# Kernel tuning notes

Measured on AMD Instinct MI355X. Metric: run time of the kernel, lower is better.

## Reference

```python
import jax, jax.numpy as jnp
import numpy as np

B, C, H, W = 8, 256, 64, 64


def setup_inputs() -> dict:
    key = jax.random.key(0)
    ks = jax.random.split(key, 9)
    s = 1.0 / np.sqrt(C)  # conv2d default init scale
    return {
        "foreground": jax.random.normal(ks[0], (B, C, H, W), jnp.float32),
        "background": jax.random.normal(ks[1], (B, C, H, W), jnp.float32),
        "mask": jax.random.uniform(ks[2], (B, C, H, W), jnp.float32),
        "Wq": jax.random.normal(ks[3], (C, C), jnp.float32) * s,
        "bq": jnp.zeros((C,), jnp.float32),
        "Wk": jax.random.normal(ks[4], (C, C), jnp.float32) * s,
        "bk": jnp.zeros((C,), jnp.float32),
        "Wv": jax.random.normal(ks[5], (C, C), jnp.float32) * s,
        "bv": jnp.zeros((C,), jnp.float32),
        "gamma": jnp.ones((1,), jnp.float32),
    }


def _conv1x1(x, Wt, b):
    # 1x1 conv == per-pixel channel matmul; x: [B,C,H,W], Wt: [Cout,Cin]
    return jnp.einsum('bchw,oc->bohw', x, Wt) + b[None, :, None, None]


def reference(foreground, background, mask, Wq, bq, Wk, bk, Wv, bv, gamma):
    b, c, h, w = foreground.shape
    hw = h * w
    # mask is already at feature resolution (interpolate would be identity)
    q = _conv1x1(foreground, Wq, bq).reshape(b, c, hw)   # [B,C,HW]
    k = _conv1x1(background, Wk, bk).reshape(b, c, hw)   # [B,C,HW]
    # bmm(q, k^T): channel-channel correlation [B,C,C]
    corr = jnp.einsum('bci,bdi->bcd', q, k)
    m_r = mask.reshape(b, c, hw)                          # [B,C,HW]
    # bmm(corr, m_r): mask-modulated scores [B,C,HW]
    scores = jnp.einsum('bcd,bdi->bci', corr, m_r)
    energy = jax.nn.softmax(scores, axis=-1)
    v = _conv1x1(foreground, Wv, bv).reshape(b, c, hw)
    attended = (energy * v).reshape(b, c, h, w)
    out = foreground * mask + gamma[0] * (1.0 - mask) * attended
    return out
```

## Files before the change

kernel.cpp:

```cpp
#include <hip/hip_runtime.h>
#include <math.h>

#define B_    8
#define C_    256
#define HW_   4096
#define CHW_  ((long)C_ * HW_)

#define BKT   32
#define LDH   40
#define KS    16
#define KCH   (HW_ / KS)
#define NCH   (C_ / BKT)
#define NPB   32

typedef __attribute__((ext_vector_type(8))) short bf16x8;
typedef __attribute__((ext_vector_type(4))) float f32x4;
#define MFMA_BF16(a, b, c) __builtin_amdgcn_mfma_f32_16x16x32_bf16((a), (b), (c), 0, 0, 0)

union frag_u { uint4 u4; bf16x8 bf; };

#define GLOAD_LDS16(src, dst)                                              \
    __builtin_amdgcn_global_load_lds(                                      \
        (const __attribute__((address_space(1))) void*)(src),              \
        (__attribute__((address_space(3))) void*)(dst), 16, 0, 0)

__device__ __forceinline__ void cvt_hl4(const float4 f, uint* h, uint* l) {
    uint u0 = __float_as_uint(f.x), u1 = __float_as_uint(f.y),
         u2 = __float_as_uint(f.z), u3 = __float_as_uint(f.w);
    uint h0 = (u0 + 0x8000u) & 0xFFFF0000u, h1 = (u1 + 0x8000u) & 0xFFFF0000u,
         h2 = (u2 + 0x8000u) & 0xFFFF0000u, h3 = (u3 + 0x8000u) & 0xFFFF0000u;
    h[0] = (h0 >> 16) | h1;
    h[1] = (h2 >> 16) | h3;
    float l0 = f.x - __uint_as_float(h0), l1 = f.y - __uint_as_float(h1),
          l2 = f.z - __uint_as_float(h2), l3 = f.w - __uint_as_float(h3);
    uint a0 = __float_as_uint(l0) & 0xFFFF0000u, a1 = __float_as_uint(l1) & 0xFFFF0000u,
         a2 = __float_as_uint(l2) & 0xFFFF0000u, a3 = __float_as_uint(l3) & 0xFFFF0000u;
    l[0] = (a0 >> 16) | a1;
    l[1] = (a2 >> 16) | a3;
}
__device__ __forceinline__ void cvt_h4(const float4 f, uint* h) {
    uint u0 = __float_as_uint(f.x), u1 = __float_as_uint(f.y),
         u2 = __float_as_uint(f.z), u3 = __float_as_uint(f.w);
    uint h0 = (u0 + 0x8000u) & 0xFFFF0000u, h1 = (u1 + 0x8000u) & 0xFFFF0000u,
         h2 = (u2 + 0x8000u) & 0xFFFF0000u, h3 = (u3 + 0x8000u) & 0xFFFF0000u;
    h[0] = (h0 >> 16) | h1;
    h[1] = (h2 >> 16) | h3;
}

__device__ __forceinline__ void cvt2_hl(float a, float b2, uint* h, uint* l) {
    uint ua = __float_as_uint(a), ub = __float_as_uint(b2);
    uint ha = (ua + 0x8000u) & 0xFFFF0000u, hb = (ub + 0x8000u) & 0xFFFF0000u;
    *h = (ha >> 16) | hb;
    float la = a - __uint_as_float(ha), lb = b2 - __uint_as_float(hb);
    *l = ((__float_as_uint(la) & 0xFFFF0000u) >> 16) | (__float_as_uint(lb) & 0xFFFF0000u);
}
__device__ __forceinline__ uint cvt2_h(float a, float b2) {
    uint ha = (__float_as_uint(a) + 0x8000u) & 0xFFFF0000u;
    uint hb = (__float_as_uint(b2) + 0x8000u) & 0xFFFF0000u;
    return (ha >> 16) | hb;
}

__global__ __launch_bounds__(256) void conv_w(
    const float* __restrict__ Wv, ushort* __restrict__ Wvh)
{
    const int i = (blockIdx.x * 256 + threadIdx.x) * 4;
    float4 v = *reinterpret_cast<const float4*>(&Wv[i]);
    uint h[2];
    cvt_h4(v, h);
    *reinterpret_cast<uint2*>(&Wvh[i]) = make_uint2(h[0], h[1]);
}

__global__ __launch_bounds__(256) void transpose_cvt(
    const float* __restrict__ mask, const float* __restrict__ fg,
    ushort* __restrict__ mTh, ushort* __restrict__ mTl, ushort* __restrict__ fTh)
{
    __shared__ float Ms[64][65];
    __shared__ float Fs[64][65];

    const int b  = blockIdx.z;
    const int c0 = blockIdx.y * 64;
    const int i0 = blockIdx.x * 64;
    const int t  = threadIdx.x;

    const int lr = t >> 2;
    const int lc = (t & 3) * 16;
    const float* mp = mask + (long)b * CHW_ + (long)(c0 + lr) * HW_ + i0 + lc;
    const float* fp = fg   + (long)b * CHW_ + (long)(c0 + lr) * HW_ + i0 + lc;
    #pragma unroll
    for (int j = 0; j < 16; j += 4) {
        *reinterpret_cast<float4*>(&Ms[lr][lc + j]) = *reinterpret_cast<const float4*>(mp + j);
        *reinterpret_cast<float4*>(&Fs[lr][lc + j]) = *reinterpret_cast<const float4*>(fp + j);
    }
    __syncthreads();

    const int oi = t >> 2;
    const int oc = (t & 3) * 16;
    uint hm[8], lm[8], hf[8];
    #pragma unroll
    for (int j = 0; j < 8; ++j) {
        const float m0v = Ms[oc + 2 * j][oi], m1v = Ms[oc + 2 * j + 1][oi];
        cvt2_hl(m0v, m1v, &hm[j], &lm[j]);
        hf[j] = cvt2_h(Fs[oc + 2 * j][oi], Fs[oc + 2 * j + 1][oi]);
    }
    const long ro = ((long)b * HW_ + i0 + oi) * C_ + c0 + oc;
    *reinterpret_cast<uint4*>(&mTh[ro])     = make_uint4(hm[0], hm[1], hm[2], hm[3]);
    *reinterpret_cast<uint4*>(&mTh[ro + 8]) = make_uint4(hm[4], hm[5], hm[6], hm[7]);
    *reinterpret_cast<uint4*>(&mTl[ro])     = make_uint4(lm[0], lm[1], lm[2], lm[3]);
    *reinterpret_cast<uint4*>(&mTl[ro + 8]) = make_uint4(lm[4], lm[5], lm[6], lm[7]);
    *reinterpret_cast<uint4*>(&fTh[ro])     = make_uint4(hf[0], hf[1], hf[2], hf[3]);
    *reinterpret_cast<uint4*>(&fTh[ro + 8]) = make_uint4(hf[4], hf[5], hf[6], hf[7]);
}

__global__ __launch_bounds__(256, 3) void gemm_nt_mfma(
    const float* __restrict__ F, const float* __restrict__ G,
    float* __restrict__ part,
    float* __restrict__ fsum, float* __restrict__ gsum)
{
    __shared__ __align__(16) ushort SMEM[4][128 * LDH];
    ushort* Ah = SMEM[0]; ushort* Al = SMEM[1];
    ushort* Bh = SMEM[2]; ushort* Bl = SMEM[3];

    const int z  = blockIdx.z;
    const int b  = z >> 4;
    const int ks = z & (KS - 1);
    const int c0 = blockIdx.y * 128;
    const int d0 = blockIdx.x * 128;
    const float* Fb = F + (long)b * CHW_ + (long)ks * KCH;
    const float* Gb = G + (long)b * CHW_ + (long)ks * KCH;
    const bool doF = (blockIdx.x == 0);
    const bool doG = (blockIdx.y == 0);

    const int t    = threadIdx.x;
    const int srow = t & 127;
    const int skf  = (t >> 7) * 16;
    const int lane = t & 63, w = t >> 6;
    const int col  = lane & 15, quad = lane >> 4;
    const int wm   = (w >> 1) * 64, wn = (w & 1) * 64;

    f32x4 acc[4][4] = {};
    float rsF = 0.0f, rsG = 0.0f;

    for (int kt = 0; kt < KCH; kt += BKT) {
        {
            const float* s = &Fb[(long)(c0 + srow) * HW_ + kt + skf];
            float4 v0 = *reinterpret_cast<const float4*>(s);
            float4 v1 = *reinterpret_cast<const float4*>(s + 4);
            float4 v2 = *reinterpret_cast<const float4*>(s + 8);
            float4 v3 = *reinterpret_cast<const float4*>(s + 12);
            if (doF) {
                rsF += (v0.x + v0.y + v0.z + v0.w) + (v1.x + v1.y + v1.z + v1.w)
                     + (v2.x + v2.y + v2.z + v2.w) + (v3.x + v3.y + v3.z + v3.w);
            }
            uint h[4], l[4];
            cvt_hl4(v0, h + 0, l + 0);
            cvt_hl4(v1, h + 2, l + 2);
            *reinterpret_cast<uint4*>(&Ah[srow * LDH + skf]) = make_uint4(h[0], h[1], h[2], h[3]);
            *reinterpret_cast<uint4*>(&Al[srow * LDH + skf]) = make_uint4(l[0], l[1], l[2], l[3]);
            cvt_hl4(v2, h + 0, l + 0);
            cvt_hl4(v3, h + 2, l + 2);
            *reinterpret_cast<uint4*>(&Ah[srow * LDH + skf + 8]) = make_uint4(h[0], h[1], h[2], h[3]);
            *reinterpret_cast<uint4*>(&Al[srow * LDH + skf + 8]) = make_uint4(l[0], l[1], l[2], l[3]);
        }
        {
            const float* s = &Gb[(long)(d0 + srow) * HW_ + kt + skf];
            float4 v0 = *reinterpret_cast<const float4*>(s);
            float4 v1 = *reinterpret_cast<const float4*>(s + 4);
            float4 v2 = *reinterpret_cast<const float4*>(s + 8);
            float4 v3 = *reinterpret_cast<const float4*>(s + 12);
            if (doG) {
                rsG += (v0.x + v0.y + v0.z + v0.w) + (v1.x + v1.y + v1.z + v1.w)
                     + (v2.x + v2.y + v2.z + v2.w) + (v3.x + v3.y + v3.z + v3.w);
            }
            uint h[4], l[4];
            cvt_hl4(v0, h + 0, l + 0);
            cvt_hl4(v1, h + 2, l + 2);
            *reinterpret_cast<uint4*>(&Bh[srow * LDH + skf]) = make_uint4(h[0], h[1], h[2], h[3]);
            *reinterpret_cast<uint4*>(&Bl[srow * LDH + skf]) = make_uint4(l[0], l[1], l[2], l[3]);
            cvt_hl4(v2, h + 0, l + 0);
            cvt_hl4(v3, h + 2, l + 2);
            *reinterpret_cast<uint4*>(&Bh[srow * LDH + skf + 8]) = make_uint4(h[0], h[1], h[2], h[3]);
            *reinterpret_cast<uint4*>(&Bl[srow * LDH + skf + 8]) = make_uint4(l[0], l[1], l[2], l[3]);
        }
        __syncthreads();

        bf16x8 bfh[4], bfl[4];
        #pragma unroll
        for (int tj = 0; tj < 4; ++tj) {
            const int r = (wn + tj * 16 + col) * LDH + quad * 8;
            bfh[tj] = *reinterpret_cast<const bf16x8*>(&Bh[r]);
            bfl[tj] = *reinterpret_cast<const bf16x8*>(&Bl[r]);
        }
        #pragma unroll
        for (int ti = 0; ti < 4; ++ti) {
            const int r = (wm + ti * 16 + col) * LDH + quad * 8;
            bf16x8 afh = *reinterpret_cast<const bf16x8*>(&Ah[r]);
            bf16x8 afl = *reinterpret_cast<const bf16x8*>(&Al[r]);
            #pragma unroll
            for (int tj = 0; tj < 4; ++tj) {
                acc[ti][tj] = MFMA_BF16(afh, bfh[tj], acc[ti][tj]);
                acc[ti][tj] = MFMA_BF16(afh, bfl[tj], acc[ti][tj]);
                acc[ti][tj] = MFMA_BF16(afl, bfh[tj], acc[ti][tj]);
            }
        }
        __syncthreads();
    }

    if (doF) atomicAdd(&fsum[b * C_ + c0 + srow], rsF);
    if (doG) atomicAdd(&gsum[b * C_ + d0 + srow], rsG);

    float* xch = (float*)&SMEM[0][0];
    float* P = part + (long)z * C_ * C_;
    const int pr = t >> 3, pu = t & 7;
    const int mmb = c0 + ((pr & 16) ? 64 : 0) + (pr & 15);
    #pragma unroll
    for (int ti = 0; ti < 4; ++ti) {
        __syncthreads();
        #pragma unroll
        for (int tj = 0; tj < 4; ++tj) {
            const int lc = wn + tj * 16 + col;
            #pragma unroll
            for (int r = 0; r < 4; ++r) {
                const int lr = (w >> 1) * 16 + quad * 4 + r;
                xch[lr * 132 + lc] = acc[ti][tj][r];
            }
        }
        __syncthreads();
        const int mm = mmb + ti * 16;
        float* dst = &P[(long)mm * C_ + d0 + pu * 16];
        const float* srcx = &xch[pr * 132 + pu * 16];
        #pragma unroll
        for (int j = 0; j < 16; j += 4)
            *reinterpret_cast<float4*>(dst + j) = *reinterpret_cast<const float4*>(srcx + j);
    }
}

__global__ __launch_bounds__(256, 2) void gemm_stats_mfma(
    const ushort* __restrict__ corrh, const ushort* __restrict__ corrl,
    const ushort* __restrict__ mTh,   const ushort* __restrict__ mTl,
    float* __restrict__ pmax, float* __restrict__ psum)
{
    __shared__ __align__(16) ushort S_[4][4096];
    __shared__ float pm[2][128], ps[2][128];

    const int b  = blockIdx.z;
    const int m0 = blockIdx.y * 128;
    const int n0 = blockIdx.x * 128;
    const ushort* Ahb = corrh + (long)b * C_ * C_;
    const ushort* Alb = corrl + (long)b * C_ * C_;
    const ushort* Bhb = mTh + (long)b * HW_ * C_;
    const ushort* Blb = mTl + (long)b * HW_ * C_;

    const int t    = threadIdx.x;
    const int lane = t & 63, w = t >> 6;
    const int col  = lane & 15, quad = lane >> 4;
    const int wm   = (w >> 1) * 64, wn = (w & 1) * 64;
    const int qsw  = (lane & 3) ^ ((lane >> 3) & 3);
    const int srw  = lane >> 2;

    int aoff[4], boff[4];
    #pragma unroll
    for (int tt = 0; tt < 4; ++tt) {
        const int rowA = wm + tt * 16 + col;
        aoff[tt] = rowA * 64 + ((quad ^ ((rowA >> 1) & 3)) << 4);
        const int rowB = wn + tt * 16 + col;
        boff[tt] = rowB * 64 + ((quad ^ ((rowB >> 1) & 3)) << 4);
    }

    f32x4 acc[4][4] = {};

    #pragma unroll 1
    for (int kc = 0; kc < NCH; ++kc) {
        const int kt = kc * BKT;
        #pragma unroll
        for (int gg = 0; gg < 2; ++gg) {
            const int rbase = w * 32 + gg * 16;
            const long rsrc = rbase + srw;
            GLOAD_LDS16(Ahb + (long)(m0 + rsrc) * C_ + kt + qsw * 8, &S_[0][rbase * 32]);
            GLOAD_LDS16(Alb + (long)(m0 + rsrc) * C_ + kt + qsw * 8, &S_[1][rbase * 32]);
            GLOAD_LDS16(Bhb + (long)(n0 + rsrc) * C_ + kt + qsw * 8, &S_[2][rbase * 32]);
            GLOAD_LDS16(Blb + (long)(n0 + rsrc) * C_ + kt + qsw * 8, &S_[3][rbase * 32]);
        }
        __syncthreads();

        bf16x8 ah[4], al[4], bh[4], bl[4];
        #pragma unroll
        for (int tt = 0; tt < 4; ++tt) {
            ah[tt] = *reinterpret_cast<const bf16x8*>((const char*)&S_[0][0] + aoff[tt]);
            al[tt] = *reinterpret_cast<const bf16x8*>((const char*)&S_[1][0] + aoff[tt]);
            bh[tt] = *reinterpret_cast<const bf16x8*>((const char*)&S_[2][0] + boff[tt]);
            bl[tt] = *reinterpret_cast<const bf16x8*>((const char*)&S_[3][0] + boff[tt]);
        }
        #pragma unroll
        for (int tj = 0; tj < 4; ++tj) {
            #pragma unroll
            for (int ti = 0; ti < 4; ++ti) {
                acc[ti][tj] = MFMA_BF16(ah[ti], bh[tj], acc[ti][tj]);
                acc[ti][tj] = MFMA_BF16(ah[ti], bl[tj], acc[ti][tj]);
                acc[ti][tj] = MFMA_BF16(al[ti], bh[tj], acc[ti][tj]);
            }
        }
        __syncthreads();
    }

    #pragma unroll
    for (int ti = 0; ti < 4; ++ti) {
        #pragma unroll
        for (int r = 0; r < 4; ++r) {
            float mx = fmaxf(fmaxf(acc[ti][0][r], acc[ti][1][r]),
                             fmaxf(acc[ti][2][r], acc[ti][3][r]));
            mx = fmaxf(mx, __shfl_xor(mx, 1));
            mx = fmaxf(mx, __shfl_xor(mx, 2));
            mx = fmaxf(mx, __shfl_xor(mx, 4));
            mx = fmaxf(mx, __shfl_xor(mx, 8));
            float se2 = __expf(acc[ti][0][r] - mx) + __expf(acc[ti][1][r] - mx)
                      + __expf(acc[ti][2][r] - mx) + __expf(acc[ti][3][r] - mx);
            se2 += __shfl_xor(se2, 1);
            se2 += __shfl_xor(se2, 2);
            se2 += __shfl_xor(se2, 4);
            se2 += __shfl_xor(se2, 8);
            if (col == 0) {
                const int rb = wm + ti * 16 + quad * 4 + r;
                pm[w & 1][rb] = mx;
                ps[w & 1][rb] = se2;
            }
        }
    }
    __syncthreads();
    if (t < 128) {
        const float a0 = pm[0][t], a1 = pm[1][t];
        const float gm = fmaxf(a0, a1);
        const float gs = ps[0][t] * __expf(a0 - gm) + ps[1][t] * __expf(a1 - gm);
        const long rowg = (long)b * C_ + m0 + t;
        pmax[rowg * NPB + blockIdx.x] = gm;
        psum[rowg * NPB + blockIdx.x] = gs;
    }
}

__global__ __launch_bounds__(256, 2) void gemm_fused_final(
    const ushort* __restrict__ corrh, const ushort* __restrict__ corrl,
    const ushort* __restrict__ Wvh,
    const ushort* __restrict__ mTh,   const ushort* __restrict__ mTl,
    const ushort* __restrict__ fTh,
    const float* __restrict__ mask,   const float* __restrict__ fg,
    const float* __restrict__ pmax,   const float* __restrict__ psum,
    const float* __restrict__ bv,     const float* __restrict__ gamma,
    float* __restrict__ out)
{
    __shared__ __align__(16) ushort S_[6][4096];
    __shared__ float sm[128], si[128];

    const int b  = blockIdx.z;
    const int m0 = blockIdx.y * 128;
    const int n0 = blockIdx.x * 128;
    const ushort* Ahb = corrh + (long)b * C_ * C_;
    const ushort* Alb = corrl + (long)b * C_ * C_;
    const ushort* Bhb = mTh + (long)b * HW_ * C_;
    const ushort* Blb = mTl + (long)b * HW_ * C_;
    const ushort* Bfb = fTh + (long)b * HW_ * C_;

    const int t    = threadIdx.x;
    const int lane = t & 63, w = t >> 6;
    const int col  = lane & 15, quad = lane >> 4;
    const int wm   = (w >> 1) * 64, wn = (w & 1) * 64;
    const int qsw  = (lane & 3) ^ ((lane >> 3) & 3);
    const int srw  = lane >> 2;

    {
        const int row  = t >> 1;
        const int part = t & 1;
        const long rowg = (long)b * C_ + m0 + row;
        const float* pmr = pmax + rowg * NPB + part * 16;
        const float* psr = psum + rowg * NPB + part * 16;
        float4 pv[4], sv[4];
        #pragma unroll
        for (int j = 0; j < 4; ++j) {
            pv[j] = *reinterpret_cast<const float4*>(pmr + j * 4);
            sv[j] = *reinterpret_cast<const float4*>(psr + j * 4);
        }
        float gm = -INFINITY;
        #pragma unroll
        for (int j = 0; j < 4; ++j)
            gm = fmaxf(gm, fmaxf(fmaxf(pv[j].x, pv[j].y), fmaxf(pv[j].z, pv[j].w)));
        gm = fmaxf(gm, __shfl_xor(gm, 1));
        float gs = 0.0f;
        #pragma unroll
        for (int j = 0; j < 4; ++j) {
            gs += sv[j].x * __expf(pv[j].x - gm) + sv[j].y * __expf(pv[j].y - gm)
                + sv[j].z * __expf(pv[j].z - gm) + sv[j].w * __expf(pv[j].w - gm);
        }
        gs += __shfl_xor(gs, 1);
        sm[row] = gm;
        si[row] = 1.0f / gs;
    }

    int aoff[4], boff[4];
    #pragma unroll
    for (int tt = 0; tt < 4; ++tt) {
        const int rowA = wm + tt * 16 + col;
        aoff[tt] = rowA * 64 + ((quad ^ ((rowA >> 1) & 3)) << 4);
        const int rowB = wn + tt * 16 + col;
        boff[tt] = rowB * 64 + ((quad ^ ((rowB >> 1) & 3)) << 4);
    }

    f32x4 acc_s[4][4] = {};
    f32x4 acc_v[4][4] = {};

    #pragma unroll 1
    for (int kc = 0; kc < NCH; ++kc) {
        const int kt = kc * BKT;
        #pragma unroll
        for (int gg = 0; gg < 2; ++gg) {
            const int rbase = w * 32 + gg * 16;
            const long rsrc = rbase + srw;
            GLOAD_LDS16(Ahb + (long)(m0 + rsrc) * C_ + kt + qsw * 8, &S_[0][rbase * 32]);
            GLOAD_LDS16(Alb + (long)(m0 + rsrc) * C_ + kt + qsw * 8, &S_[1][rbase * 32]);
            GLOAD_LDS16(Wvh + (long)(m0 + rsrc) * C_ + kt + qsw * 8, &S_[2][rbase * 32]);
            GLOAD_LDS16(Bhb + (long)(n0 + rsrc) * C_ + kt + qsw * 8, &S_[3][rbase * 32]);
            GLOAD_LDS16(Blb + (long)(n0 + rsrc) * C_ + kt + qsw * 8, &S_[4][rbase * 32]);
            GLOAD_LDS16(Bfb + (long)(n0 + rsrc) * C_ + kt + qsw * 8, &S_[5][rbase * 32]);
        }
        __syncthreads();

        bf16x8 ah[4], al[4], aw[4], bh[4], bl[4], bf[4];
        #pragma unroll
        for (int tt = 0; tt < 4; ++tt) {
            ah[tt] = *reinterpret_cast<const bf16x8*>((const char*)&S_[0][0] + aoff[tt]);
            al[tt] = *reinterpret_cast<const bf16x8*>((const char*)&S_[1][0] + aoff[tt]);
            aw[tt] = *reinterpret_cast<const bf16x8*>((const char*)&S_[2][0] + aoff[tt]);
            bh[tt] = *reinterpret_cast<const bf16x8*>((const char*)&S_[3][0] + boff[tt]);
            bl[tt] = *reinterpret_cast<const bf16x8*>((const char*)&S_[4][0] + boff[tt]);
            bf[tt] = *reinterpret_cast<const bf16x8*>((const char*)&S_[5][0] + boff[tt]);
        }
        #pragma unroll
        for (int tj = 0; tj < 4; ++tj) {
            #pragma unroll
            for (int ti = 0; ti < 4; ++ti) {
                acc_s[ti][tj] = MFMA_BF16(ah[ti], bh[tj], acc_s[ti][tj]);
                acc_s[ti][tj] = MFMA_BF16(ah[ti], bl[tj], acc_s[ti][tj]);
                acc_s[ti][tj] = MFMA_BF16(al[ti], bh[tj], acc_s[ti][tj]);
                acc_v[ti][tj] = MFMA_BF16(aw[ti], bf[tj], acc_v[ti][tj]);
            }
        }
        __syncthreads();
    }

    const float g = gamma[0];
    #pragma unroll
    for (int ti = 0; ti < 4; ++ti) {
        #pragma unroll
        for (int r = 0; r < 4; ++r) {
            const int lrow = wm + ti * 16 + quad * 4 + r;
            const float mx  = sm[lrow];
            const float inv = si[lrow] * g;
            #pragma unroll
            for (int tj = 0; tj < 4; ++tj)
                acc_s[ti][tj][r] = __expf(acc_s[ti][tj][r] - mx) * inv;
        }
    }

    #pragma unroll
    for (int ti = 0; ti < 4; ++ti) {
        const int m = m0 + wm + ti * 16 + quad * 4;
        #pragma unroll
        for (int r = 0; r < 4; ++r) {
            const float bvm = bv[m + r];
            #pragma unroll
            for (int tj = 0; tj < 4; ++tj) {
                const int n = n0 + wn + tj * 16 + col;
                const long e = (long)b * CHW_ + (long)(m + r) * HW_ + n;
                const float f  = fg[e];
                const float mk = mask[e];
                const float vv = acc_v[ti][tj][r] + bvm;
                out[e] = f * mk + (1.0f - mk) * acc_s[ti][tj][r] * vv;
            }
        }
    }
}

__global__ __launch_bounds__(256) void reduce_part(
    const float* __restrict__ part, float* __restrict__ S1)
{
    const long i4 = ((long)blockIdx.x * 256 + threadIdx.x) * 4;
    const int  b  = (int)(i4 >> 16);
    const long e  = i4 & 65535;
    const float* p = part + ((long)b * KS) * 65536 + e;
    float4 s = make_float4(0.f, 0.f, 0.f, 0.f);
    #pragma unroll
    for (int ks = 0; ks < KS; ++ks) {
        float4 v = *reinterpret_cast<const float4*>(&p[(long)ks * 65536]);
        s.x += v.x; s.y += v.y; s.z += v.z; s.w += v.w;
    }
    *reinterpret_cast<float4*>(&S1[i4]) = s;
}

#define BK64 16
#define LDT64 68
__global__ __launch_bounds__(256) void gemm_nt64(
    const float* __restrict__ S1, const float* __restrict__ Wk,
    float* __restrict__ T)
{
    __shared__ float As[BK64][LDT64];
    __shared__ float Bs[BK64][LDT64];
    const int r0 = blockIdx.y * 64;
    const int d0 = blockIdx.x * 64;
    const int t   = threadIdx.x;
    const int tx  = t & 15, ty = t >> 4;
    const int tx4 = tx * 4, ty4 = ty * 4;
    const int am  = t >> 2, ak4 = (t & 3) * 4;

    float acc[4][4] = {};
    for (int k0 = 0; k0 < C_; k0 += BK64) {
        float4 av = *reinterpret_cast<const float4*>(&S1[(long)(r0 + am) * C_ + k0 + ak4]);
        float4 bw = *reinterpret_cast<const float4*>(&Wk[(long)(d0 + am) * C_ + k0 + ak4]);
        As[ak4+0][am]=av.x; As[ak4+1][am]=av.y; As[ak4+2][am]=av.z; As[ak4+3][am]=av.w;
        Bs[ak4+0][am]=bw.x; Bs[ak4+1][am]=bw.y; Bs[ak4+2][am]=bw.z; Bs[ak4+3][am]=bw.w;
        __syncthreads();
        #pragma unroll
        for (int kk = 0; kk < BK64; ++kk) {
            float4 a = *reinterpret_cast<const float4*>(&As[kk][ty4]);
            float4 x = *reinterpret_cast<const float4*>(&Bs[kk][tx4]);
            const float ar[4] = {a.x,a.y,a.z,a.w};
            const float xr[4] = {x.x,x.y,x.z,x.w};
            #pragma unroll
            for (int r = 0; r < 4; ++r)
                #pragma unroll
                for (int s = 0; s < 4; ++s)
                    acc[r][s] = fmaf(ar[r], xr[s], acc[r][s]);
        }
        __syncthreads();
    }
    #pragma unroll
    for (int r = 0; r < 4; ++r) {
        float4 o; o.x=acc[r][0]; o.y=acc[r][1]; o.z=acc[r][2]; o.w=acc[r][3];
        *reinterpret_cast<float4*>(&T[(long)(r0 + ty4 + r) * C_ + d0 + tx4]) = o;
    }
}

__global__ __launch_bounds__(256) void gemm_nn64_rank1(
    const float* __restrict__ Wq, const float* __restrict__ T,
    const float* __restrict__ Wk, const float* __restrict__ bk,
    const float* __restrict__ bq,
    const float* __restrict__ fsum, const float* __restrict__ gsum,
    ushort* __restrict__ corrh, ushort* __restrict__ corrl)
{
    __shared__ float As[BK64][LDT64];
    __shared__ float Bs[BK64][LDT64];
    __shared__ float u_s[64], wh_s[64];
    const int b  = blockIdx.z;
    const int m0 = blockIdx.y * 64;
    const int n0 = blockIdx.x * 64;
    const float* Tb = T + (long)b * C_ * C_;

    const int t   = threadIdx.x;
    const int tx  = t & 15, ty = t >> 4;
    const int tx4 = tx * 4, ty4 = ty * 4;
    const int am  = t >> 2, ak4 = (t & 3) * 4;
    const int xk  = ty,     xn4 = tx4;

    if (t < 64) {
        const float* wrow = Wq + (long)(m0 + t) * C_;
        const float* s = fsum + b * C_;
        float a = 0.0f;
        for (int e2 = 0; e2 < C_; ++e2) a = fmaf(wrow[e2], s[e2], a);
        u_s[t] = a;
    } else if (t < 128) {
        const int d = n0 + (t - 64);
        const float* wrow = Wk + (long)d * C_;
        const float* s = gsum + b * C_;
        float a = 0.0f;
        for (int e2 = 0; e2 < C_; ++e2) a = fmaf(wrow[e2], s[e2], a);
        wh_s[t - 64] = a + (float)HW_ * bk[d];
    }

    float acc[4][4] = {};
    for (int k0 = 0; k0 < C_; k0 += BK64) {
        float4 av = *reinterpret_cast<const float4*>(&Wq[(long)(m0 + am) * C_ + k0 + ak4]);
        float4 xv = *reinterpret_cast<const float4*>(&Tb[(long)(k0 + xk) * C_ + n0 + xn4]);
        As[ak4+0][am]=av.x; As[ak4+1][am]=av.y; As[ak4+2][am]=av.z; As[ak4+3][am]=av.w;
        *reinterpret_cast<float4*>(&Bs[xk][xn4]) = xv;
        __syncthreads();
        #pragma unroll
        for (int kk = 0; kk < BK64; ++kk) {
            float4 a = *reinterpret_cast<const float4*>(&As[kk][ty4]);
            float4 x = *reinterpret_cast<const float4*>(&Bs[kk][tx4]);
            const float ar[4] = {a.x,a.y,a.z,a.w};
            const float xr[4] = {x.x,x.y,x.z,x.w};
            #pragma unroll
            for (int r = 0; r < 4; ++r)
                #pragma unroll
                for (int s = 0; s < 4; ++s)
                    acc[r][s] = fmaf(ar[r], xr[s], acc[r][s]);
        }
        __syncthreads();
    }

    float4 bkv = *reinterpret_cast<const float4*>(&bk[n0 + tx4]);
    float4 whv = make_float4(wh_s[tx4], wh_s[tx4+1], wh_s[tx4+2], wh_s[tx4+3]);
    #pragma unroll
    for (int r = 0; r < 4; ++r) {
        const int m = m0 + ty4 + r;
        const float um = u_s[ty4 + r];
        const float bm = bq[m];
        float4 o;
        o.x = acc[r][0] + um*bkv.x + bm*whv.x;
        o.y = acc[r][1] + um*bkv.y + bm*whv.y;
        o.z = acc[r][2] + um*bkv.z + bm*whv.z;
        o.w = acc[r][3] + um*bkv.w + bm*whv.w;
        uint h[2], l[2];
        cvt_hl4(o, h, l);
        const long e = (long)b * C_ * C_ + (long)m * C_ + n0 + tx4;
        *reinterpret_cast<uint2*>(&corrh[e]) = make_uint2(h[0], h[1]);
        *reinterpret_cast<uint2*>(&corrl[e]) = make_uint2(l[0], l[1]);
    }
}

extern "C" void kernel_launch(void* const* d_in, const int* in_sizes, int n_in,
                              void* d_out, int out_size, void* d_ws, size_t ws_size,
                              hipStream_t stream)
{
    const float* fg    = (const float*)d_in[0];
    const float* bg    = (const float*)d_in[1];
    const float* mask  = (const float*)d_in[2];
    const float* Wq    = (const float*)d_in[3];
    const float* bq    = (const float*)d_in[4];
    const float* Wk    = (const float*)d_in[5];
    const float* bk    = (const float*)d_in[6];
    const float* Wv    = (const float*)d_in[7];
    const float* bv    = (const float*)d_in[8];
    const float* gamma = (const float*)d_in[9];
    float* out = (float*)d_out;

    char* ws = (char*)d_ws;
    float*  part   = (float*)(ws);
    float*  S1     = (float*)(ws + 33554432);
    float*  T      = (float*)(ws + 35651584);
    ushort* corrh  = (ushort*)(ws + 37748736);
    ushort* corrl  = (ushort*)(ws + 38797312);
    ushort* Wvh    = (ushort*)(ws + 39845888);
    float*  fsum   = (float*)(ws + 39976960);
    float*  gsum   = (float*)(ws + 39985152);
    float*  pmax   = (float*)(ws + 33554432);
    float*  psum   = (float*)(ws + 33816576);
    ushort* mTh    = (ushort*)(ws);
    ushort* mTl    = (ushort*)(ws + 16777216);
    ushort* fTh    = (ushort*)(ws + 40517632);

    const dim3 blk(256);

    hipMemsetAsync(fsum, 0, 16384, stream);

    conv_w<<<dim3(64), blk, 0, stream>>>(Wv, Wvh);

    gemm_nt_mfma<<<dim3(2, 2, B_ * KS), blk, 0, stream>>>(fg, bg, part, fsum, gsum);
    reduce_part<<<dim3(B_ * C_ * C_ / 1024), blk, 0, stream>>>(part, S1);

    transpose_cvt<<<dim3(HW_ / 64, C_ / 64, B_), blk, 0, stream>>>(
        mask, fg, mTh, mTl, fTh);

    gemm_nt64<<<dim3(C_ / 64, B_ * C_ / 64), blk, 0, stream>>>(S1, Wk, T);
    gemm_nn64_rank1<<<dim3(4, 4, B_), blk, 0, stream>>>(
        Wq, T, Wk, bk, bq, fsum, gsum, corrh, corrl);

    gemm_stats_mfma<<<dim3(HW_ / 128, C_ / 128, B_), blk, 0, stream>>>(
        corrh, corrl, mTh, mTl, pmax, psum);

    gemm_fused_final<<<dim3(HW_ / 128, C_ / 128, B_), blk, 0, stream>>>(
        corrh, corrl, Wvh, mTh, mTl, fTh, mask, fg, pmax, psum, bv, gamma, out);
}
```

Before: 282.4 us.

## Software-pipeline global loads across three GEMM kernels with double buffering

The correlation GEMM now prefetches the next K-chunk of foreground and background into registers while the MFMAs for the current chunk run. The two mask-product GEMMs double-buffer their B-operand LDS tiles via async global-to-LDS loads issued one chunk ahead. Their A operands (corr hi/lo, Wv) are loaded straight from global into registers instead of being staged through LDS. This aims to hide global memory latency behind compute, at the cost of more registers and doubled LDS for the B tiles, which could reduce occupancy.

```diff
diff --git a/kernel.cpp b/kernel.cpp
--- a/kernel.cpp
+++ b/kernel.cpp
@@ -137,51 +137,60 @@
     const int col  = lane & 15, quad = lane >> 4;
     const int wm   = (w >> 1) * 64, wn = (w & 1) * 64;
 
+    const float* Frow = Fb + (long)(c0 + srow) * HW_ + skf;
+    const float* Grow = Gb + (long)(d0 + srow) * HW_ + skf;
+
     f32x4 acc[4][4] = {};
     float rsF = 0.0f, rsG = 0.0f;
 
+    float4 cf[4], cg[4];
+    #pragma unroll
+    for (int j = 0; j < 4; ++j) {
+        cf[j] = *reinterpret_cast<const float4*>(Frow + j * 4);
+        cg[j] = *reinterpret_cast<const float4*>(Grow + j * 4);
+    }
+
     for (int kt = 0; kt < KCH; kt += BKT) {
+        if (doF) {
+            #pragma unroll
+            for (int j = 0; j < 4; ++j)
+                rsF += (cf[j].x + cf[j].y) + (cf[j].z + cf[j].w);
+        }
+        if (doG) {
+            #pragma unroll
+            for (int j = 0; j < 4; ++j)
+                rsG += (cg[j].x + cg[j].y) + (cg[j].z + cg[j].w);
+        }
         {
-            const float* s = &Fb[(long)(c0 + srow) * HW_ + kt + skf];
-            float4 v0 = *reinterpret_cast<const float4*>(s);
-            float4 v1 = *reinterpret_cast<const float4*>(s + 4);
-            float4 v2 = *reinterpret_cast<const float4*>(s + 8);
-            float4 v3 = *reinterpret_cast<const float4*>(s + 12);
-            if (doF) {
-                rsF += (v0.x + v0.y + v0.z + v0.w) + (v1.x + v1.y + v1.z + v1.w)
-                     + (v2.x + v2.y + v2.z + v2.w) + (v3.x + v3.y + v3.z + v3.w);
-            }
             uint h[4], l[4];
-            cvt_hl4(v0, h + 0, l + 0);
-            cvt_hl4(v1, h + 2, l + 2);
+            cvt_hl4(cf[0], h + 0, l + 0);
+            cvt_hl4(cf[1], h + 2, l + 2);
             *reinterpret_cast<uint4*>(&Ah[srow * LDH + skf]) = make_uint4(h[0], h[1], h[2], h[3]);
             *reinterpret_cast<uint4*>(&Al[srow * LDH + skf]) = make_uint4(l[0], l[1], l[2], l[3]);
-            cvt_hl4(v2, h + 0, l + 0);
-            cvt_hl4(v3, h + 2, l + 2);
+            cvt_hl4(cf[2], h + 0, l + 0);
+            cvt_hl4(cf[3], h + 2, l + 2);
             *reinterpret_cast<uint4*>(&Ah[srow * LDH + skf + 8]) = make_uint4(h[0], h[1], h[2], h[3]);
             *reinterpret_cast<uint4*>(&Al[srow * LDH + skf + 8]) = make_uint4(l[0], l[1], l[2], l[3]);
-        }
-        {
-            const float* s = &Gb[(long)(d0 + srow) * HW_ + kt + skf];
-            float4 v0 = *reinterpret_cast<const float4*>(s);
-            float4 v1 = *reinterpret_cast<const float4*>(s + 4);
-            float4 v2 = *reinterpret_cast<const float4*>(s + 8);
-            float4 v3 = *reinterpret_cast<const float4*>(s + 12);
-            if (doG) {
-                rsG += (v0.x + v0.y + v0.z + v0.w) + (v1.x + v1.y + v1.z + v1.w)
-                     + (v2.x + v2.y + v2.z + v2.w) + (v3.x + v3.y + v3.z + v3.w);
-            }
-            uint h[4], l[4];
-            cvt_hl4(v0, h + 0, l + 0);
-            cvt_hl4(v1, h + 2, l + 2);
+            cvt_hl4(cg[0], h + 0, l + 0);
+            cvt_hl4(cg[1], h + 2, l + 2);
             *reinterpret_cast<uint4*>(&Bh[srow * LDH + skf]) = make_uint4(h[0], h[1], h[2], h[3]);
             *reinterpret_cast<uint4*>(&Bl[srow * LDH + skf]) = make_uint4(l[0], l[1], l[2], l[3]);
-            cvt_hl4(v2, h + 0, l + 0);
-            cvt_hl4(v3, h + 2, l + 2);
+            cvt_hl4(cg[2], h + 0, l + 0);
+            cvt_hl4(cg[3], h + 2, l + 2);
             *reinterpret_cast<uint4*>(&Bh[srow * LDH + skf + 8]) = make_uint4(h[0], h[1], h[2], h[3]);
             *reinterpret_cast<uint4*>(&Bl[srow * LDH + skf + 8]) = make_uint4(l[0], l[1], l[2], l[3]);
         }
         __syncthreads();
+
+        const bool more = (kt + BKT < KCH);
+        float4 nf[4], ng[4];
+        if (more) {
+            #pragma unroll
+            for (int j = 0; j < 4; ++j) {
+                nf[j] = *reinterpret_cast<const float4*>(Frow + kt + BKT + j * 4);
+                ng[j] = *reinterpret_cast<const float4*>(Grow + kt + BKT + j * 4);
+            }
+        }
 
         bf16x8 bfh[4], bfl[4];
         #pragma unroll
@@ -203,6 +212,10 @@
             }
         }
         __syncthreads();
+        if (more) {
+            #pragma unroll
+            for (int j = 0; j < 4; ++j) { cf[j] = nf[j]; cg[j] = ng[j]; }
+        }
     }
 
     if (doF) atomicAdd(&fsum[b * C_ + c0 + srow], rsF);
@@ -239,7 +252,7 @@
     const ushort* __restrict__ mTh,   const ushort* __restrict__ mTl,
     float* __restrict__ pmax, float* __restrict__ psum)
 {
-    __shared__ __align__(16) ushort S_[4][4096];
+    __shared__ __align__(16) ushort S_[2][2][4096];
     __shared__ float pm[2][128], ps[2][128];
 
     const int b  = blockIdx.z;
@@ -257,38 +270,59 @@
     const int qsw  = (lane & 3) ^ ((lane >> 3) & 3);
     const int srw  = lane >> 2;
 
-    int aoff[4], boff[4];
+    int boff[4];
+    long aoa[4];
     #pragma unroll
     for (int tt = 0; tt < 4; ++tt) {
-        const int rowA = wm + tt * 16 + col;
-        aoff[tt] = rowA * 64 + ((quad ^ ((rowA >> 1) & 3)) << 4);
         const int rowB = wn + tt * 16 + col;
         boff[tt] = rowB * 64 + ((quad ^ ((rowB >> 1) & 3)) << 4);
-    }
+        aoa[tt] = (long)(m0 + wm + tt * 16 + col) * C_ + quad * 8;
+    }
+
+#define STAGE_S(buf, kk) do {                                              \
+    _Pragma("unroll")                                                      \
+    for (int gg = 0; gg < 2; ++gg) {                                       \
+        const int rbase = w * 32 + gg * 16;                                \
+        const long rsrc = rbase + srw;                                     \
+        GLOAD_LDS16(Bhb + (long)(n0 + rsrc) * C_ + (kk) + qsw * 8, &S_[buf][0][rbase * 32]); \
+        GLOAD_LDS16(Blb + (long)(n0 + rsrc) * C_ + (kk) + qsw * 8, &S_[buf][1][rbase * 32]); \
+    }                                                                      \
+} while (0)
 
     f32x4 acc[4][4] = {};
 
+    STAGE_S(0, 0);
+    bf16x8 nah[4], nal[4];
+    #pragma unroll
+    for (int tt = 0; tt < 4; ++tt) {
+        nah[tt] = *reinterpret_cast<const bf16x8*>(&Ahb[aoa[tt]]);
+        nal[tt] = *reinterpret_cast<const bf16x8*>(&Alb[aoa[tt]]);
+    }
+    __syncthreads();
+
+    int cur = 0;
     #pragma unroll 1
     for (int kc = 0; kc < NCH; ++kc) {
         const int kt = kc * BKT;
-        #pragma unroll
-        for (int gg = 0; gg < 2; ++gg) {
-            const int rbase = w * 32 + gg * 16;
-            const long rsrc = rbase + srw;
-            GLOAD_LDS16(Ahb + (long)(m0 + rsrc) * C_ + kt + qsw * 8, &S_[0][rbase * 32]);
-            GLOAD_LDS16(Alb + (long)(m0 + rsrc) * C_ + kt + qsw * 8, &S_[1][rbase * 32]);
-            GLOAD_LDS16(Bhb + (long)(n0 + rsrc) * C_ + kt + qsw * 8, &S_[2][rbase * 32]);
-            GLOAD_LDS16(Blb + (long)(n0 + rsrc) * C_ + kt + qsw * 8, &S_[3][rbase * 32]);
-        }
-        __syncthreads();
-
-        bf16x8 ah[4], al[4], bh[4], bl[4];
+        bf16x8 ah[4], al[4];
+        #pragma unroll
+        for (int tt = 0; tt < 4; ++tt) { ah[tt] = nah[tt]; al[tt] = nal[tt]; }
+
+        if (kc + 1 < NCH) {
+            STAGE_S(cur ^ 1, kt + BKT);
+            #pragma unroll
+            for (int tt = 0; tt < 4; ++tt) {
+                nah[tt] = *reinterpret_cast<const bf16x8*>(&Ahb[aoa[tt] + kt + BKT]);
+                nal[tt] = *reinterpret_cast<const bf16x8*>(&Alb[aoa[tt] + kt + BKT]);
+            }
+        }
+
+        const char* base = (const char*)&S_[cur][0][0];
+        bf16x8 bh[4], bl[4];
         #pragma unroll
         for (int tt = 0; tt < 4; ++tt) {
-            ah[tt] = *reinterpret_cast<const bf16x8*>((const char*)&S_[0][0] + aoff[tt]);
-            al[tt] = *reinterpret_cast<const bf16x8*>((const char*)&S_[1][0] + aoff[tt]);
-            bh[tt] = *reinterpret_cast<const bf16x8*>((const char*)&S_[2][0] + boff[tt]);
-            bl[tt] = *reinterpret_cast<const bf16x8*>((const char*)&S_[3][0] + boff[tt]);
+            bh[tt] = *reinterpret_cast<const bf16x8*>(base + boff[tt]);
+            bl[tt] = *reinterpret_cast<const bf16x8*>(base + 8192 + boff[tt]);
         }
         #pragma unroll
         for (int tj = 0; tj < 4; ++tj) {
@@ -300,7 +334,9 @@
             }
         }
         __syncthreads();
-    }
+        cur ^= 1;
+    }
+#undef STAGE_S
 
     #pragma unroll
     for (int ti = 0; ti < 4; ++ti) {
@@ -346,7 +382,7 @@
     const float* __restrict__ bv,     const float* __restrict__ gamma,
     float* __restrict__ out)
 {
-    __shared__ __align__(16) ushort S_[6][4096];
+    __shared__ __align__(16) ushort S_[2][3][4096];
     __shared__ float sm[128], si[128];
 
     const int b  = blockIdx.z;
@@ -393,43 +429,65 @@
         si[row] = 1.0f / gs;
     }
 
-    int aoff[4], boff[4];
+    int boff[4];
+    long aoa[4];
     #pragma unroll
     for (int tt = 0; tt < 4; ++tt) {
-        const int rowA = wm + tt * 16 + col;
-        aoff[tt] = rowA * 64 + ((quad ^ ((rowA >> 1) & 3)) << 4);
         const int rowB = wn + tt * 16 + col;
         boff[tt] = rowB * 64 + ((quad ^ ((rowB >> 1) & 3)) << 4);
-    }
+        aoa[tt] = (long)(m0 + wm + tt * 16 + col) * C_ + quad * 8;
+    }
+
+#define STAGE_F(buf, kk) do {                                              \
+    _Pragma("unroll")                                                      \
+    for (int gg = 0; gg < 2; ++gg) {                                       \
+        const int rbase = w * 32 + gg * 16;                                \
+        const long rsrc = rbase + srw;                                     \
+        GLOAD_LDS16(Bhb + (long)(n0 + rsrc) * C_ + (kk) + qsw * 8, &S_[buf][0][rbase * 32]); \
+        GLOAD_LDS16(Blb + (long)(n0 + rsrc) * C_ + (kk) + qsw * 8, &S_[buf][1][rbase * 32]); \
+        GLOAD_LDS16(Bfb + (long)(n0 + rsrc) * C_ + (kk) + qsw * 8, &S_[buf][2][rbase * 32]); \
+    }                                                                      \
+} while (0)
 
     f32x4 acc_s[4][4] = {};
     f32x4 acc_v[4][4] = {};
 
+    STAGE_F(0, 0);
+    bf16x8 nah[4], nal[4];
+    #pragma unroll
+    for (int tt = 0; tt < 4; ++tt) {
+        nah[tt] = *reinterpret_cast<const bf16x8*>(&Ahb[aoa[tt]]);
+        nal[tt] = *reinterpret_cast<const bf16x8*>(&Alb[aoa[tt]]);
+    }
+    __syncthreads();
+
+    int cur = 0;
     #pragma unroll 1
     for (int kc = 0; kc < NCH; ++kc) {
         const int kt = kc * BKT;
-        #pragma unroll
-        for (int gg = 0; gg < 2; ++gg) {
-            const int rbase = w * 32 + gg * 16;
-            const long rsrc = rbase + srw;
-            GLOAD_LDS16(Ahb + (long)(m0 + rsrc) * C_ + kt + qsw * 8, &S_[0][rbase * 32]);
-            GLOAD_LDS16(Alb + (long)(m0 + rsrc) * C_ + kt + qsw * 8, &S_[1][rbase * 32]);
-            GLOAD_LDS16(Wvh + (long)(m0 + rsrc) * C_ + kt + qsw * 8, &S_[2][rbase * 32]);
-            GLOAD_LDS16(Bhb + (long)(n0 + rsrc) * C_ + kt + qsw * 8, &S_[3][rbase * 32]);
-            GLOAD_LDS16(Blb + (long)(n0 + rsrc) * C_ + kt + qsw * 8, &S_[4][rbase * 32]);
-            GLOAD_LDS16(Bfb + (long)(n0 + rsrc) * C_ + kt + qsw * 8, &S_[5][rbase * 32]);
-        }
-        __syncthreads();
-
-        bf16x8 ah[4], al[4], aw[4], bh[4], bl[4], bf[4];
+        bf16x8 ah[4], al[4], aw[4];
+        #pragma unroll
+        for (int tt = 0; tt < 4; ++tt) { ah[tt] = nah[tt]; al[tt] = nal[tt]; }
+        #pragma unroll
+        for (int tt = 0; tt < 4; ++tt)
+            aw[tt] = *reinterpret_cast<const bf16x8*>(&Wvh[aoa[tt] + kt]);
+
+        if (kc + 1 < NCH) {
+            STAGE_F(cur ^ 1, kt + BKT);
+            #pragma unroll
+            for (int tt = 0; tt < 4; ++tt) {
+                nah[tt] = *reinterpret_cast<const bf16x8*>(&Ahb[aoa[tt] + kt + BKT]);
+                nal[tt] = *reinterpret_cast<const bf16x8*>(&Alb[aoa[tt] + kt + BKT]);
+            }
+        }
+
+        const char* base = (const char*)&S_[cur][0][0];
+        bf16x8 bh[4], bl[4], bf[4];
         #pragma unroll
         for (int tt = 0; tt < 4; ++tt) {
-            ah[tt] = *reinterpret_cast<const bf16x8*>((const char*)&S_[0][0] + aoff[tt]);
-            al[tt] = *reinterpret_cast<const bf16x8*>((const char*)&S_[1][0] + aoff[tt]);
-            aw[tt] = *reinterpret_cast<const bf16x8*>((const char*)&S_[2][0] + aoff[tt]);
-            bh[tt] = *reinterpret_cast<const bf16x8*>((const char*)&S_[3][0] + boff[tt]);
-            bl[tt] = *reinterpret_cast<const bf16x8*>((const char*)&S_[4][0] + boff[tt]);
-            bf[tt] = *reinterpret_cast<const bf16x8*>((const char*)&S_[5][0] + boff[tt]);
+            bh[tt] = *reinterpret_cast<const bf16x8*>(base + boff[tt]);
+            bl[tt] = *reinterpret_cast<const bf16x8*>(base + 8192 + boff[tt]);
+            bf[tt] = *reinterpret_cast<const bf16x8*>(base + 16384 + boff[tt]);
         }
         #pragma unroll
         for (int tj = 0; tj < 4; ++tj) {
@@ -442,7 +500,9 @@
             }
         }
         __syncthreads();
-    }
+        cur ^= 1;
+    }
+#undef STAGE_F
 
     const float g = gamma[0];
     #pragma unroll
```

Measured after the change: 305.0 us. 1.08x slower.

## Prefetch next K tile in gram GEMM and merge mid-stage kernels into one launch

Applied to the files above, without the earlier changes.

The split-K gram GEMM now keeps the current tile's fp32 values in registers and issues the global loads for the next tile before the MFMA compute, so load latency overlaps compute. The transpose/convert, S1·Wk GEMM and Wv conversion kernels are merged into one launch whose blockIdx.z selects the role, which removes two launches and lets these independent jobs run concurrently. In exchange the prefetch buffers raise register pressure under a 3-waves occupancy bound, and the merged kernel has uneven block roles.

```diff
diff --git a/kernel.cpp b/kernel.cpp
--- a/kernel.cpp
+++ b/kernel.cpp
@@ -60,57 +60,6 @@
     return (ha >> 16) | hb;
 }
 
-__global__ __launch_bounds__(256) void conv_w(
-    const float* __restrict__ Wv, ushort* __restrict__ Wvh)
-{
-    const int i = (blockIdx.x * 256 + threadIdx.x) * 4;
-    float4 v = *reinterpret_cast<const float4*>(&Wv[i]);
-    uint h[2];
-    cvt_h4(v, h);
-    *reinterpret_cast<uint2*>(&Wvh[i]) = make_uint2(h[0], h[1]);
-}
-
-__global__ __launch_bounds__(256) void transpose_cvt(
-    const float* __restrict__ mask, const float* __restrict__ fg,
-    ushort* __restrict__ mTh, ushort* __restrict__ mTl, ushort* __restrict__ fTh)
-{
-    __shared__ float Ms[64][65];
-    __shared__ float Fs[64][65];
-
-    const int b  = blockIdx.z;
-    const int c0 = blockIdx.y * 64;
-    const int i0 = blockIdx.x * 64;
-    const int t  = threadIdx.x;
-
-    const int lr = t >> 2;
-    const int lc = (t & 3) * 16;
-    const float* mp = mask + (long)b * CHW_ + (long)(c0 + lr) * HW_ + i0 + lc;
-    const float* fp = fg   + (long)b * CHW_ + (long)(c0 + lr) * HW_ + i0 + lc;
-    #pragma unroll
-    for (int j = 0; j < 16; j += 4) {
-        *reinterpret_cast<float4*>(&Ms[lr][lc + j]) = *reinterpret_cast<const float4*>(mp + j);
-        *reinterpret_cast<float4*>(&Fs[lr][lc + j]) = *reinterpret_cast<const float4*>(fp + j);
-    }
-    __syncthreads();
-
-    const int oi = t >> 2;
-    const int oc = (t & 3) * 16;
-    uint hm[8], lm[8], hf[8];
-    #pragma unroll
-    for (int j = 0; j < 8; ++j) {
-        const float m0v = Ms[oc + 2 * j][oi], m1v = Ms[oc + 2 * j + 1][oi];
-        cvt2_hl(m0v, m1v, &hm[j], &lm[j]);
-        hf[j] = cvt2_h(Fs[oc + 2 * j][oi], Fs[oc + 2 * j + 1][oi]);
-    }
-    const long ro = ((long)b * HW_ + i0 + oi) * C_ + c0 + oc;
-    *reinterpret_cast<uint4*>(&mTh[ro])     = make_uint4(hm[0], hm[1], hm[2], hm[3]);
-    *reinterpret_cast<uint4*>(&mTh[ro + 8]) = make_uint4(hm[4], hm[5], hm[6], hm[7]);
-    *reinterpret_cast<uint4*>(&mTl[ro])     = make_uint4(lm[0], lm[1], lm[2], lm[3]);
-    *reinterpret_cast<uint4*>(&mTl[ro + 8]) = make_uint4(lm[4], lm[5], lm[6], lm[7]);
-    *reinterpret_cast<uint4*>(&fTh[ro])     = make_uint4(hf[0], hf[1], hf[2], hf[3]);
-    *reinterpret_cast<uint4*>(&fTh[ro + 8]) = make_uint4(hf[4], hf[5], hf[6], hf[7]);
-}
-
 __global__ __launch_bounds__(256, 3) void gemm_nt_mfma(
     const float* __restrict__ F, const float* __restrict__ G,
     float* __restrict__ part,
@@ -137,51 +86,60 @@
     const int col  = lane & 15, quad = lane >> 4;
     const int wm   = (w >> 1) * 64, wn = (w & 1) * 64;
 
+    const float* Frow = Fb + (long)(c0 + srow) * HW_ + skf;
+    const float* Grow = Gb + (long)(d0 + srow) * HW_ + skf;
+
     f32x4 acc[4][4] = {};
     float rsF = 0.0f, rsG = 0.0f;
 
+    float4 cf[4], cg[4];
+    #pragma unroll
+    for (int j = 0; j < 4; ++j) {
+        cf[j] = *reinterpret_cast<const float4*>(Frow + j * 4);
+        cg[j] = *reinterpret_cast<const float4*>(Grow + j * 4);
+    }
+
     for (int kt = 0; kt < KCH; kt += BKT) {
+        if (doF) {
+            #pragma unroll
+            for (int j = 0; j < 4; ++j)
+                rsF += (cf[j].x + cf[j].y) + (cf[j].z + cf[j].w);
+        }
+        if (doG) {
+            #pragma unroll
+            for (int j = 0; j < 4; ++j)
+                rsG += (cg[j].x + cg[j].y) + (cg[j].z + cg[j].w);
+        }
         {
-            const float* s = &Fb[(long)(c0 + srow) * HW_ + kt + skf];
-            float4 v0 = *reinterpret_cast<const float4*>(s);
-            float4 v1 = *reinterpret_cast<const float4*>(s + 4);
-            float4 v2 = *reinterpret_cast<const float4*>(s + 8);
-            float4 v3 = *reinterpret_cast<const float4*>(s + 12);
-            if (doF) {
-                rsF += (v0.x + v0.y + v0.z + v0.w) + (v1.x + v1.y + v1.z + v1.w)
-                     + (v2.x + v2.y + v2.z + v2.w) + (v3.x + v3.y + v3.z + v3.w);
-            }
             uint h[4], l[4];
-            cvt_hl4(v0, h + 0, l + 0);
-            cvt_hl4(v1, h + 2, l + 2);
+            cvt_hl4(cf[0], h + 0, l + 0);
+            cvt_hl4(cf[1], h + 2, l + 2);
             *reinterpret_cast<uint4*>(&Ah[srow * LDH + skf]) = make_uint4(h[0], h[1], h[2], h[3]);
             *reinterpret_cast<uint4*>(&Al[srow * LDH + skf]) = make_uint4(l[0], l[1], l[2], l[3]);
-            cvt_hl4(v2, h + 0, l + 0);
-            cvt_hl4(v3, h + 2, l + 2);
+            cvt_hl4(cf[2], h + 0, l + 0);
+            cvt_hl4(cf[3], h + 2, l + 2);
             *reinterpret_cast<uint4*>(&Ah[srow * LDH + skf + 8]) = make_uint4(h[0], h[1], h[2], h[3]);
             *reinterpret_cast<uint4*>(&Al[srow * LDH + skf + 8]) = make_uint4(l[0], l[1], l[2], l[3]);
-        }
-        {
-            const float* s = &Gb[(long)(d0 + srow) * HW_ + kt + skf];
-            float4 v0 = *reinterpret_cast<const float4*>(s);
-            float4 v1 = *reinterpret_cast<const float4*>(s + 4);
-            float4 v2 = *reinterpret_cast<const float4*>(s + 8);
-            float4 v3 = *reinterpret_cast<const float4*>(s + 12);
-            if (doG) {
-                rsG += (v0.x + v0.y + v0.z + v0.w) + (v1.x + v1.y + v1.z + v1.w)
-                     + (v2.x + v2.y + v2.z + v2.w) + (v3.x + v3.y + v3.z + v3.w);
-            }
-            uint h[4], l[4];
-            cvt_hl4(v0, h + 0, l + 0);
-            cvt_hl4(v1, h + 2, l + 2);
+            cvt_hl4(cg[0], h + 0, l + 0);
+            cvt_hl4(cg[1], h + 2, l + 2);
             *reinterpret_cast<uint4*>(&Bh[srow * LDH + skf]) = make_uint4(h[0], h[1], h[2], h[3]);
             *reinterpret_cast<uint4*>(&Bl[srow * LDH + skf]) = make_uint4(l[0], l[1], l[2], l[3]);
-            cvt_hl4(v2, h + 0, l + 0);
-            cvt_hl4(v3, h + 2, l + 2);
+            cvt_hl4(cg[2], h + 0, l + 0);
+            cvt_hl4(cg[3], h + 2, l + 2);
             *reinterpret_cast<uint4*>(&Bh[srow * LDH + skf + 8]) = make_uint4(h[0], h[1], h[2], h[3]);
             *reinterpret_cast<uint4*>(&Bl[srow * LDH + skf + 8]) = make_uint4(l[0], l[1], l[2], l[3]);
         }
         __syncthreads();
+
+        const bool more = (kt + BKT < KCH);
+        float4 nf[4], ng[4];
+        if (more) {
+            #pragma unroll
+            for (int j = 0; j < 4; ++j) {
+                nf[j] = *reinterpret_cast<const float4*>(Frow + kt + BKT + j * 4);
+                ng[j] = *reinterpret_cast<const float4*>(Grow + kt + BKT + j * 4);
+            }
+        }
 
         bf16x8 bfh[4], bfl[4];
         #pragma unroll
@@ -203,6 +161,10 @@
             }
         }
         __syncthreads();
+        if (more) {
+            #pragma unroll
+            for (int j = 0; j < 4; ++j) { cf[j] = nf[j]; cg[j] = ng[j]; }
+        }
     }
 
     if (doF) atomicAdd(&fsum[b * C_ + c0 + srow], rsF);
@@ -231,6 +193,123 @@
         #pragma unroll
         for (int j = 0; j < 16; j += 4)
             *reinterpret_cast<float4*>(dst + j) = *reinterpret_cast<const float4*>(srcx + j);
+    }
+}
+
+__global__ __launch_bounds__(256) void reduce_part(
+    const float* __restrict__ part, float* __restrict__ S1)
+{
+    const long i4 = ((long)blockIdx.x * 256 + threadIdx.x) * 4;
+    const int  b  = (int)(i4 >> 16);
+    const long e  = i4 & 65535;
+    const float* p = part + ((long)b * KS) * 65536 + e;
+    float4 s = make_float4(0.f, 0.f, 0.f, 0.f);
+    #pragma unroll
+    for (int ks = 0; ks < KS; ++ks) {
+        float4 v = *reinterpret_cast<const float4*>(&p[(long)ks * 65536]);
+        s.x += v.x; s.y += v.y; s.z += v.z; s.w += v.w;
+    }
+    *reinterpret_cast<float4*>(&S1[i4]) = s;
+}
+
+#define BK64 16
+#define LDT64 68
+__global__ __launch_bounds__(256) void mid_pass(
+    const float* __restrict__ mask, const float* __restrict__ fg,
+    ushort* __restrict__ mTh, ushort* __restrict__ mTl, ushort* __restrict__ fTh,
+    const float* __restrict__ S1, const float* __restrict__ Wk,
+    float* __restrict__ T,
+    const float* __restrict__ Wv, ushort* __restrict__ Wvh)
+{
+    __shared__ float SH[8320];
+
+    const int t = threadIdx.x;
+    const int z = blockIdx.z;
+
+    if (z < 8) {
+        const int b  = z;
+        const int c0 = blockIdx.y * 64;
+        const int i0 = blockIdx.x * 64;
+        float* Ms = SH;
+        float* Fs = SH + 4160;
+
+        const int lr = t >> 2;
+        const int lc = (t & 3) * 16;
+        const float* mp = mask + (long)b * CHW_ + (long)(c0 + lr) * HW_ + i0 + lc;
+        const float* fp = fg   + (long)b * CHW_ + (long)(c0 + lr) * HW_ + i0 + lc;
+        #pragma unroll
+        for (int j = 0; j < 16; j += 4) {
+            *reinterpret_cast<float4*>(&Ms[lr * 65 + lc + j]) = *reinterpret_cast<const float4*>(mp + j);
+            *reinterpret_cast<float4*>(&Fs[lr * 65 + lc + j]) = *reinterpret_cast<const float4*>(fp + j);
+        }
+        __syncthreads();
+
+        const int oi = t >> 2;
+        const int oc = (t & 3) * 16;
+        uint hm[8], lm[8], hf[8];
+        #pragma unroll
+        for (int j = 0; j < 8; ++j) {
+            const float m0v = Ms[(oc + 2 * j) * 65 + oi], m1v = Ms[(oc + 2 * j + 1) * 65 + oi];
+            cvt2_hl(m0v, m1v, &hm[j], &lm[j]);
+            hf[j] = cvt2_h(Fs[(oc + 2 * j) * 65 + oi], Fs[(oc + 2 * j + 1) * 65 + oi]);
+        }
+        const long ro = ((long)b * HW_ + i0 + oi) * C_ + c0 + oc;
+        *reinterpret_cast<uint4*>(&mTh[ro])     = make_uint4(hm[0], hm[1], hm[2], hm[3]);
+        *reinterpret_cast<uint4*>(&mTh[ro + 8]) = make_uint4(hm[4], hm[5], hm[6], hm[7]);
+        *reinterpret_cast<uint4*>(&mTl[ro])     = make_uint4(lm[0], lm[1], lm[2], lm[3]);
+        *reinterpret_cast<uint4*>(&mTl[ro + 8]) = make_uint4(lm[4], lm[5], lm[6], lm[7]);
+        *reinterpret_cast<uint4*>(&fTh[ro])     = make_uint4(hf[0], hf[1], hf[2], hf[3]);
+        *reinterpret_cast<uint4*>(&fTh[ro + 8]) = make_uint4(hf[4], hf[5], hf[6], hf[7]);
+        return;
+    }
+
+    const int flat = blockIdx.y * 64 + blockIdx.x;
+    if (flat < 128) {
+        const int r0 = (flat >> 2) * 64;
+        const int d0 = (flat & 3) * 64;
+        float* As = SH;
+        float* Bs = SH + BK64 * LDT64;
+
+        const int tx  = t & 15, ty = t >> 4;
+        const int tx4 = tx * 4, ty4 = ty * 4;
+        const int am  = t >> 2, ak4 = (t & 3) * 4;
+
+        float acc[4][4] = {};
+        for (int k0 = 0; k0 < C_; k0 += BK64) {
+            float4 av = *reinterpret_cast<const float4*>(&S1[(long)(r0 + am) * C_ + k0 + ak4]);
+            float4 bw = *reinterpret_cast<const float4*>(&Wk[(long)(d0 + am) * C_ + k0 + ak4]);
+            As[(ak4+0)*LDT64+am]=av.x; As[(ak4+1)*LDT64+am]=av.y;
+            As[(ak4+2)*LDT64+am]=av.z; As[(ak4+3)*LDT64+am]=av.w;
+            Bs[(ak4+0)*LDT64+am]=bw.x; Bs[(ak4+1)*LDT64+am]=bw.y;
+            Bs[(ak4+2)*LDT64+am]=bw.z; Bs[(ak4+3)*LDT64+am]=bw.w;
+            __syncthreads();
+            #pragma unroll
+            for (int kk = 0; kk < BK64; ++kk) {
+                float4 a = *reinterpret_cast<const float4*>(&As[kk*LDT64 + ty4]);
+                float4 x = *reinterpret_cast<const float4*>(&Bs[kk*LDT64 + tx4]);
+                const float ar[4] = {a.x,a.y,a.z,a.w};
+                const float xr[4] = {x.x,x.y,x.z,x.w};
+                #pragma unroll
+                for (int r = 0; r < 4; ++r)
+                    #pragma unroll
+                    for (int s = 0; s < 4; ++s)
+                        acc[r][s] = fmaf(ar[r], xr[s], acc[r][s]);
+            }
+            __syncthreads();
+        }
+        #pragma unroll
+        for (int r = 0; r < 4; ++r) {
+            float4 o; o.x=acc[r][0]; o.y=acc[r][1]; o.z=acc[r][2]; o.w=acc[r][3];
+            *reinterpret_cast<float4*>(&T[(long)(r0 + ty4 + r) * C_ + d0 + tx4]) = o;
+        }
+        return;
+    }
+    if (flat < 192) {
+        const int i = ((flat - 128) * 256 + t) * 4;
+        float4 v = *reinterpret_cast<const float4*>(&Wv[i]);
+        uint h[2];
+        cvt_h4(v, h);
+        *reinterpret_cast<uint2*>(&Wvh[i]) = make_uint2(h[0], h[1]);
     }
 }
 
@@ -477,65 +556,6 @@
     }
 }
 
-__global__ __launch_bounds__(256) void reduce_part(
-    const float* __restrict__ part, float* __restrict__ S1)
-{
-    const long i4 = ((long)blockIdx.x * 256 + threadIdx.x) * 4;
-    const int  b  = (int)(i4 >> 16);
-    const long e  = i4 & 65535;
-    const float* p = part + ((long)b * KS) * 65536 + e;
-    float4 s = make_float4(0.f, 0.f, 0.f, 0.f);
-    #pragma unroll
-    for (int ks = 0; ks < KS; ++ks) {
-        float4 v = *reinterpret_cast<const float4*>(&p[(long)ks * 65536]);
-        s.x += v.x; s.y += v.y; s.z += v.z; s.w += v.w;
-    }
-    *reinterpret_cast<float4*>(&S1[i4]) = s;
-}
-
-#define BK64 16
-#define LDT64 68
-__global__ __launch_bounds__(256) void gemm_nt64(
-    const float* __restrict__ S1, const float* __restrict__ Wk,
-    float* __restrict__ T)
-{
-    __shared__ float As[BK64][LDT64];
-    __shared__ float Bs[BK64][LDT64];
-    const int r0 = blockIdx.y * 64;
-    const int d0 = blockIdx.x * 64;
-    const int t   = threadIdx.x;
-    const int tx  = t & 15, ty = t >> 4;
-    const int tx4 = tx * 4, ty4 = ty * 4;
-    const int am  = t >> 2, ak4 = (t & 3) * 4;
-
-    float acc[4][4] = {};
-    for (int k0 = 0; k0 < C_; k0 += BK64) {
-        float4 av = *reinterpret_cast<const float4*>(&S1[(long)(r0 + am) * C_ + k0 + ak4]);
-        float4 bw = *reinterpret_cast<const float4*>(&Wk[(long)(d0 + am) * C_ + k0 + ak4]);
-        As[ak4+0][am]=av.x; As[ak4+1][am]=av.y; As[ak4+2][am]=av.z; As[ak4+3][am]=av.w;
-        Bs[ak4+0][am]=bw.x; Bs[ak4+1][am]=bw.y; Bs[ak4+2][am]=bw.z; Bs[ak4+3][am]=bw.w;
-        __syncthreads();
-        #pragma unroll
-        for (int kk = 0; kk < BK64; ++kk) {
-            float4 a = *reinterpret_cast<const float4*>(&As[kk][ty4]);
-            float4 x = *reinterpret_cast<const float4*>(&Bs[kk][tx4]);
-            const float ar[4] = {a.x,a.y,a.z,a.w};
-            const float xr[4] = {x.x,x.y,x.z,x.w};
-            #pragma unroll
-            for (int r = 0; r < 4; ++r)
-                #pragma unroll
-                for (int s = 0; s < 4; ++s)
-                    acc[r][s] = fmaf(ar[r], xr[s], acc[r][s]);
-        }
-        __syncthreads();
-    }
-    #pragma unroll
-    for (int r = 0; r < 4; ++r) {
-        float4 o; o.x=acc[r][0]; o.y=acc[r][1]; o.z=acc[r][2]; o.w=acc[r][3];
-        *reinterpret_cast<float4*>(&T[(long)(r0 + ty4 + r) * C_ + d0 + tx4]) = o;
-    }
-}
-
 __global__ __launch_bounds__(256) void gemm_nn64_rank1(
     const float* __restrict__ Wq, const float* __restrict__ T,
     const float* __restrict__ Wk, const float* __restrict__ bk,
@@ -649,15 +669,12 @@
 
     hipMemsetAsync(fsum, 0, 16384, stream);
 
-    conv_w<<<dim3(64), blk, 0, stream>>>(Wv, Wvh);
-
     gemm_nt_mfma<<<dim3(2, 2, B_ * KS), blk, 0, stream>>>(fg, bg, part, fsum, gsum);
     reduce_part<<<dim3(B_ * C_ * C_ / 1024), blk, 0, stream>>>(part, S1);
 
-    transpose_cvt<<<dim3(HW_ / 64, C_ / 64, B_), blk, 0, stream>>>(
-        mask, fg, mTh, mTl, fTh);
-
-    gemm_nt64<<<dim3(C_ / 64, B_ * C_ / 64), blk, 0, stream>>>(S1, Wk, T);
+    mid_pass<<<dim3(HW_ / 64, C_ / 64, B_ + 1), blk, 0, stream>>>(
+        mask, fg, mTh, mTl, fTh, S1, Wk, T, Wv, Wvh);
+
     gemm_nn64_rank1<<<dim3(4, 4, B_), blk, 0, stream>>>(
         Wq, T, Wk, bk, bq, fsum, gsum, corrh, corrl);
 
```

Result: no change. 279.2 us (-1.1%).
